# Kernel tuning notes

Hardware: AMD Instinct MI355X
Metric: run time of the kernel (lower is better)

The kernel has to match this reference:

```python
import jax, jax.numpy as jnp
import numpy as np

EPS_VAR = 1e-10
EPS_PERP = 1e-07


def setup_inputs() -> dict:
    key = jax.random.key(0)
    k1, k2 = jax.random.split(key, 2)
    bs, dim_z, W, H, K = 64, 64, 32, 32, 1024
    z_from_encoder = jax.random.normal(k1, (bs, dim_z, W, H), dtype=jnp.float32)
    codebook = jax.random.normal(k2, (K, dim_z), dtype=jnp.float32)
    var_q = jnp.ones((1,), dtype=jnp.float32)
    return {"z_from_encoder": z_from_encoder, "var_q": var_q, "codebook": codebook}


def _vq_forward(z_from_encoder, var_q, codebook):
    bs, dim_z, W, H = z_from_encoder.shape
    K = codebook.shape[0]
    # precision = 1 / clamp(var_q, min=1e-10); gaussian_1 -> global scalar weight
    precision_q = 1.0 / jnp.clip(var_q, EPS_VAR)
    weight = (0.5 * precision_q).reshape(())  # scalar

    # [bs, dim_z, W, H] -> [N, dim_z], N = bs*W*H
    z_flat = jnp.transpose(z_from_encoder, (0, 2, 3, 1)).reshape(-1, dim_z)

    # squared euclidean distance to every code: ||z||^2 + ||c||^2 - 2 z c^T  -> [N, K]
    d2 = (jnp.sum(z_flat * z_flat, axis=1, keepdims=True)
          + jnp.sum(codebook * codebook, axis=1)
          - 2.0 * (z_flat @ codebook.T))
    logit = -(weight * d2)

    log_probs = jax.nn.log_softmax(logit, axis=-1)   # [N, K]
    probs = jnp.exp(log_probs)                        # [N, K]

    # deterministic quantization: argmax -> gather codebook (== one_hot @ codebook)
    indices = jnp.argmax(logit, axis=1)               # [N]
    z_q = codebook[indices].reshape(bs, W, H, dim_z)
    z_to_decoder = jnp.transpose(z_q, (0, 3, 1, 2))   # [bs, dim_z, W, H]

    # avg_probs = mean of hard one-hot encodings (histogram of code usage)
    N = indices.shape[0]
    avg_probs = jnp.zeros((K,), dtype=logit.dtype).at[indices].add(1.0) / N

    # kld_discrete = sum(probs * log_probs) / bs  (sum over N and K)
    kld_discrete = jnp.sum(probs * log_probs) / bs
    # kld_continuous = mean over batch of sum_i weight * (z - z_q)^2
    diff2 = (z_from_encoder - z_to_decoder) ** 2
    kld_continuous = jnp.mean(jnp.sum(weight * diff2, axis=(1, 2, 3)))
    loss = kld_discrete + kld_continuous

    perplexity = jnp.exp(-jnp.sum(avg_probs * jnp.log(avg_probs + EPS_PERP)))
    return z_to_decoder, loss, perplexity


def reference(z_from_encoder, var_q, codebook):
    return _vq_forward(z_from_encoder, var_q, codebook)
```

## Files before the change

### kernel.cpp

```cpp
#include <hip/hip_runtime.h>

#define WS_CNORM_B  512
#define WS_COUNTS_B 4608
#define WS_CBHI_B   8704

typedef __attribute__((ext_vector_type(8))) short short8;
typedef __attribute__((ext_vector_type(4))) float f32x4;

__device__ __forceinline__ unsigned short f2bf(float x) {
  unsigned u = __builtin_bit_cast(unsigned, x);
  u += 0x7fffu + ((u >> 16) & 1u);
  return (unsigned short)(u >> 16);
}
__device__ __forceinline__ int qw(int r, int d) {
  return (r << 6) | (d ^ (r & 31));
}

__global__ __launch_bounds__(256) void vq_prep(const float* __restrict__ cb,
                                               char* __restrict__ ws) {
  int tid = blockIdx.x * 256 + threadIdx.x;
  unsigned* w32 = (unsigned*)ws;
  if (tid < 128) w32[tid] = 0u;
  if (tid < 1024) w32[1152 + tid] = 0u;
  int k = tid >> 6;
  float v = cb[tid];
  ((unsigned short*)(ws + WS_CBHI_B))[tid] = f2bf(v);
  float s = v * v;
  #pragma unroll
  for (int o = 32; o > 0; o >>= 1) s += __shfl_down(s, o);
  if ((threadIdx.x & 63) == 0) ((float*)(ws + WS_CNORM_B))[k] = s;
}

#define ST_OFF   16384
#define FIDX_OFF 17664

__global__ __launch_bounds__(256, 4) void vq_main(const float* __restrict__ z,
                                                  const float* __restrict__ cb,
                                                  const float* __restrict__ var_q,
                                                  char* __restrict__ ws,
                                                  float* __restrict__ out) {
  __shared__ __align__(16) char smem[17920];

  const int t = threadIdx.x;
  const int b = blockIdx.x;
  const int bb = b >> 4, p0 = (b & 15) << 6;
  const int l = t & 63, wv = t >> 6;
  const int lg = l >> 4, lr = l & 15;
  const float w = 0.5f / fmaxf(var_q[0], 1e-10f);
  const float w2 = 2.f * w;
  const float nw = -w;

  for (int i = 0; i < 8; ++i) {
    int idx = t + i * 256;
    int d2 = idx >> 6, p = idx & 63;
    float v0 = z[bb * 65536 + (2 * d2) * 1024 + p0 + p];
    float v1 = z[bb * 65536 + (2 * d2 + 1) * 1024 + p0 + p];
    unsigned short h0 = f2bf(v0), h1 = f2bf(v1);
    int byte = (p * 128 + d2 * 4) ^ ((p & 7) << 4);
    *(unsigned*)(smem + byte) = ((unsigned)h1 << 16) | h0;
  }
  __syncthreads();

  short8 a_hi[2];
  {
    int row = wv * 16 + lr;
    #pragma unroll
    for (int ks = 0; ks < 2; ++ks) {
      int byte = (row * 128 + ks * 64 + lg * 16) ^ ((row & 7) << 4);
      a_hi[ks] = *(const short8*)(smem + byte);
    }
  }
  __syncthreads();

  const char* cbh = ws + WS_CBHI_B;
  {
    #pragma unroll
    for (int pas = 0; pas < 2; ++pas) {
      int o = t + pas * 256;
      int dst = (o * 16) ^ (((o >> 3) & 7) << 4);
      *(f32x4*)(smem + dst) = *(const f32x4*)(cbh + o * 16);
    }
  }
  __syncthreads();

  float m[4], S1[4], S2[4], b1[4], b2[4];
  #pragma unroll
  for (int j = 0; j < 4; ++j) {
    m[j] = -1e30f; S1[j] = 0.f; S2[j] = 0.f; b1[j] = -1e30f; b2[j] = -1e30f;
  }

  const float* cnf = (const float*)(ws + WS_CNORM_B);

  for (int ch = 0; ch < 16; ++ch) {
    char* cur = smem + (ch & 1) * 8192;
    char* nxt = smem + ((ch + 1) & 1) * 8192;
    f32x4 rh0, rh1;
    const bool pf = ch < 15;
    if (pf) {
      const char* sh = cbh + (ch + 1) * 8192 + t * 16;
      rh0 = *(const f32x4*)sh;
      rh1 = *(const f32x4*)(sh + 4096);
    }
    float cn2[4];
    #pragma unroll
    for (int ct = 0; ct < 4; ++ct) cn2[ct] = nw * cnf[ch * 64 + ct * 16 + lr];

    f32x4 acc[4];
    #pragma unroll
    for (int ct = 0; ct < 4; ++ct) {
      f32x4 a = {};
      #pragma unroll
      for (int ks = 0; ks < 2; ++ks) {
        int cr = ct * 16 + lr;
        int byte = (cr * 128 + ks * 64 + lg * 16) ^ ((cr & 7) << 4);
        short8 bh = *(const short8*)(cur + byte);
        a = __builtin_amdgcn_mfma_f32_16x16x32_bf16(a_hi[ks], bh, a, 0, 0, 0);
      }
      acc[ct] = a;
    }

    #pragma unroll
    for (int j = 0; j < 4; ++j) {
      float lv[4];
      #pragma unroll
      for (int ct = 0; ct < 4; ++ct) lv[ct] = fmaf(acc[ct][j], w2, cn2[ct]);
      float lm = fmaxf(fmaxf(lv[0], lv[1]), fmaxf(lv[2], lv[3]));
      float mn = fmaxf(m[j], lm);
      float sc = __expf(m[j] - mn);
      S1[j] *= sc; S2[j] *= sc; m[j] = mn;
      #pragma unroll
      for (int ct = 0; ct < 4; ++ct) {
        float x = lv[ct];
        unsigned ku = (unsigned)(ch * 64 + ct * 16 + lr);
        unsigned xb = (__builtin_bit_cast(unsigned, x) & ~1023u) | ku;
        float xp = __builtin_bit_cast(float, xb);
        float tm = fminf(b1[j], xp);
        b1[j] = fmaxf(b1[j], xp);
        b2[j] = fmaxf(b2[j], tm);
        float e = __expf(x - mn);
        S1[j] += e;
        S2[j] = fmaf(x, e, S2[j]);
      }
    }

    if (pf) {
      #pragma unroll
      for (int pas = 0; pas < 2; ++pas) {
        int o = t + pas * 256;
        int dst = (o * 16) ^ (((o >> 3) & 7) << 4);
        *(f32x4*)(nxt + dst) = pas ? rh1 : rh0;
      }
    }
    __syncthreads();
  }

  #pragma unroll
  for (int st = 1; st < 16; st <<= 1) {
    #pragma unroll
    for (int j = 0; j < 4; ++j) {
      float om = __shfl_xor(m[j], st);
      float o1 = __shfl_xor(S1[j], st);
      float o2 = __shfl_xor(S2[j], st);
      float ov1 = __shfl_xor(b1[j], st);
      float ov2 = __shfl_xor(b2[j], st);
      float mn = fmaxf(m[j], om);
      float sa = __expf(m[j] - mn), sb = __expf(om - mn);
      S1[j] = sa * S1[j] + sb * o1;
      S2[j] = sa * S2[j] + sb * o2;
      m[j] = mn;
      float nb1 = fmaxf(b1[j], ov1);
      float nb2 = fmaxf(fminf(b1[j], ov1), fmaxf(b2[j], ov2));
      b1[j] = nb1; b2[j] = nb2;
    }
  }

  float* stw = (float*)(smem + ST_OFF);
  if (lr == 0) {
    #pragma unroll
    for (int j = 0; j < 4; ++j) {
      int r = wv * 16 + lg * 4 + j;
      float* p = stw + r * 5;
      p[0] = m[j]; p[1] = S1[j]; p[2] = S2[j]; p[3] = b1[j]; p[4] = b2[j];
    }
  }
  __syncthreads();

  int* fidx = (int*)(smem + FIDX_OFF);
  float rowent = 0.f, d2min = 0.f;
  if (t < 64) {
    const float* p = stw + t * 5;
    float mn = p[0], s1 = p[1], s2 = p[2];
    int ka = (int)(__builtin_bit_cast(unsigned, p[3]) & 1023u);
    int kb = (int)(__builtin_bit_cast(unsigned, p[4]) & 1023u);
    rowent = (s2 - mn * s1) / s1 - __logf(s1);
    const float* zp = z + bb * 65536 + p0 + t;
    const float* c1p = cb + ka * 64;
    const float* c2p = cb + kb * 64;
    float zn = 0.f, d1 = 0.f, d2 = 0.f;
    #pragma unroll 4
    for (int d4 = 0; d4 < 16; ++d4) {
      f32x4 ca = *(const f32x4*)(c1p + d4 * 4);
      f32x4 cc = *(const f32x4*)(c2p + d4 * 4);
      #pragma unroll
      for (int e = 0; e < 4; ++e) {
        float v = zp[(d4 * 4 + e) * 1024];
        zn = fmaf(v, v, zn);
        d1 = fmaf(v, ca[e], d1);
        d2 = fmaf(v, cc[e], d2);
      }
    }
    float da = zn + cnf[ka] - 2.f * d1;
    float db = zn + cnf[kb] - 2.f * d2;
    int kwin; float dwin;
    if (da < db || (da == db && ka < kb)) { kwin = ka; dwin = da; }
    else { kwin = kb; dwin = db; }
    fidx[t] = kwin;
    d2min = dwin;
    atomicAdd((unsigned*)(ws + WS_COUNTS_B) + kwin, 1u);
  }
  #pragma unroll
  for (int o = 32; o > 0; o >>= 1) {
    rowent += __shfl_down(rowent, o);
    d2min += __shfl_down(d2min, o);
  }
  if (t == 0) {
    float* wsf = (float*)ws;
    int slot = b & 63;
    atomicAdd(&wsf[slot * 2], rowent);
    atomicAdd(&wsf[slot * 2 + 1], d2min);
  }
  __syncthreads();

  float* zl = (float*)smem;
  for (int i = 0; i < 16; ++i) {
    int idx = t + i * 256;
    int r = idx >> 6, d = idx & 63;
    zl[qw(r, d)] = cb[fidx[r] * 64 + d];
  }
  __syncthreads();
  float* outz = out + bb * 65536 + p0;
  #pragma unroll
  for (int i = 0; i < 4; ++i) {
    int q = t + i * 256;
    int d = q >> 4, rq = q & 15, r = rq << 2;
    f32x4 v;
    v.x = zl[qw(r + 0, d)];
    v.y = zl[qw(r + 1, d)];
    v.z = zl[qw(r + 2, d)];
    v.w = zl[qw(r + 3, d)];
    *(f32x4*)&outz[d * 1024 + r] = v;
  }
}

__global__ __launch_bounds__(1024) void vq_finalize(const float* __restrict__ var_q,
                                                    char* __restrict__ ws,
                                                    float* __restrict__ out) {
  __shared__ float red[48];
  int t = threadIdx.x;
  const unsigned* counts = (const unsigned*)(ws + WS_COUNTS_B);
  const float* wsf = (const float*)ws;
  float avg = (float)counts[t] * (1.0f / 65536.0f);
  float term = avg * __logf(avg + 1e-7f);
  float pd = 0.f, pc = 0.f;
  if (t < 64) { pd = wsf[2 * t]; pc = wsf[2 * t + 1]; }
  #pragma unroll
  for (int o = 32; o > 0; o >>= 1) {
    term += __shfl_down(term, o);
    pd += __shfl_down(pd, o);
    pc += __shfl_down(pc, o);
  }
  int wv = t >> 6, lane = t & 63;
  if (lane == 0) { red[wv * 3] = term; red[wv * 3 + 1] = pd; red[wv * 3 + 2] = pc; }
  __syncthreads();
  if (t == 0) {
    float ts = 0.f, ps = 0.f, cs = 0.f;
    #pragma unroll
    for (int i = 0; i < 16; ++i) {
      ts += red[i * 3]; ps += red[i * 3 + 1]; cs += red[i * 3 + 2];
    }
    float w = 0.5f / fmaxf(var_q[0], 1e-10f);
    out[4194304] = ps / 64.f + w * cs / 64.f;
    out[4194305] = __expf(-ts);
  }
}

extern "C" void kernel_launch(void* const* d_in, const int* in_sizes, int n_in,
                              void* d_out, int out_size, void* d_ws, size_t ws_size,
                              hipStream_t stream) {
  const float* z = (const float*)d_in[0];
  const float* vq = (const float*)d_in[1];
  const float* cb = (const float*)d_in[2];
  float* out = (float*)d_out;
  char* ws = (char*)d_ws;

  vq_prep<<<256, 256, 0, stream>>>(cb, ws);
  vq_main<<<1024, 256, 0, stream>>>(z, cb, vq, ws, out);
  vq_finalize<<<1, 1024, 0, stream>>>(vq, ws, out);
}
```

Before: 58.12 us.

## Split codebook across two half-blocks of 512 threads and merge softmax stats

Doubles the block size to 512 threads. Each half of the block scans half of the codebook (512 codes) for the same 64 pixels, using its own double-buffered shared-memory region. The online-softmax and top-2 statistics from the two halves are merged at the end. This halves the serial chunk loop per block and adds parallelism, at the cost of twice the shared memory per block, an extra merge step, and tighter register limits from launch_bounds(512,8).

```diff
diff --git a/kernel.cpp b/kernel.cpp
--- a/kernel.cpp
+++ b/kernel.cpp
@@ -31,27 +31,29 @@
   if ((threadIdx.x & 63) == 0) ((float*)(ws + WS_CNORM_B))[k] = s;
 }
 
-#define ST_OFF   16384
-#define FIDX_OFF 17664
-
-__global__ __launch_bounds__(256, 4) void vq_main(const float* __restrict__ z,
+#define ST_OFF   32768
+#define FIDX_OFF 35328
+
+__global__ __launch_bounds__(512, 8) void vq_main(const float* __restrict__ z,
                                                   const float* __restrict__ cb,
                                                   const float* __restrict__ var_q,
                                                   char* __restrict__ ws,
                                                   float* __restrict__ out) {
-  __shared__ __align__(16) char smem[17920];
+  __shared__ __align__(16) char smem[35584];
 
   const int t = threadIdx.x;
   const int b = blockIdx.x;
   const int bb = b >> 4, p0 = (b & 15) << 6;
-  const int l = t & 63, wv = t >> 6;
+  const int half = t >> 8, th = t & 255;
+  const int wv = t >> 6, wq = wv & 3;
+  const int l = t & 63;
   const int lg = l >> 4, lr = l & 15;
   const float w = 0.5f / fmaxf(var_q[0], 1e-10f);
   const float w2 = 2.f * w;
   const float nw = -w;
 
-  for (int i = 0; i < 8; ++i) {
-    int idx = t + i * 256;
+  for (int i = 0; i < 4; ++i) {
+    int idx = t + i * 512;
     int d2 = idx >> 6, p = idx & 63;
     float v0 = z[bb * 65536 + (2 * d2) * 1024 + p0 + p];
     float v1 = z[bb * 65536 + (2 * d2 + 1) * 1024 + p0 + p];
@@ -63,7 +65,7 @@
 
   short8 a_hi[2];
   {
-    int row = wv * 16 + lr;
+    int row = wq * 16 + lr;
     #pragma unroll
     for (int ks = 0; ks < 2; ++ks) {
       int byte = (row * 128 + ks * 64 + lg * 16) ^ ((row & 7) << 4);
@@ -72,13 +74,14 @@
   }
   __syncthreads();
 
-  const char* cbh = ws + WS_CBHI_B;
+  const char* cbh = ws + WS_CBHI_B + half * 65536;
+  char* hbase = smem + half * 16384;
   {
     #pragma unroll
     for (int pas = 0; pas < 2; ++pas) {
-      int o = t + pas * 256;
+      int o = th + pas * 256;
       int dst = (o * 16) ^ (((o >> 3) & 7) << 4);
-      *(f32x4*)(smem + dst) = *(const f32x4*)(cbh + o * 16);
+      *(f32x4*)(hbase + dst) = *(const f32x4*)(cbh + o * 16);
     }
   }
   __syncthreads();
@@ -91,19 +94,20 @@
 
   const float* cnf = (const float*)(ws + WS_CNORM_B);
 
-  for (int ch = 0; ch < 16; ++ch) {
-    char* cur = smem + (ch & 1) * 8192;
-    char* nxt = smem + ((ch + 1) & 1) * 8192;
+  for (int ch = 0; ch < 8; ++ch) {
+    char* cur = hbase + (ch & 1) * 8192;
+    char* nxt = hbase + ((ch + 1) & 1) * 8192;
     f32x4 rh0, rh1;
-    const bool pf = ch < 15;
+    const bool pf = ch < 7;
     if (pf) {
-      const char* sh = cbh + (ch + 1) * 8192 + t * 16;
+      const char* sh = cbh + (ch + 1) * 8192 + th * 16;
       rh0 = *(const f32x4*)sh;
       rh1 = *(const f32x4*)(sh + 4096);
     }
     float cn2[4];
     #pragma unroll
-    for (int ct = 0; ct < 4; ++ct) cn2[ct] = nw * cnf[ch * 64 + ct * 16 + lr];
+    for (int ct = 0; ct < 4; ++ct)
+      cn2[ct] = nw * cnf[half * 512 + ch * 64 + ct * 16 + lr];
 
     f32x4 acc[4];
     #pragma unroll
@@ -131,7 +135,7 @@
       #pragma unroll
       for (int ct = 0; ct < 4; ++ct) {
         float x = lv[ct];
-        unsigned ku = (unsigned)(ch * 64 + ct * 16 + lr);
+        unsigned ku = (unsigned)(half * 512 + ch * 64 + ct * 16 + lr);
         unsigned xb = (__builtin_bit_cast(unsigned, x) & ~1023u) | ku;
         float xp = __builtin_bit_cast(float, xb);
         float tm = fminf(b1[j], xp);
@@ -146,7 +150,7 @@
     if (pf) {
       #pragma unroll
       for (int pas = 0; pas < 2; ++pas) {
-        int o = t + pas * 256;
+        int o = th + pas * 256;
         int dst = (o * 16) ^ (((o >> 3) & 7) << 4);
         *(f32x4*)(nxt + dst) = pas ? rh1 : rh0;
       }
@@ -178,8 +182,8 @@
   if (lr == 0) {
     #pragma unroll
     for (int j = 0; j < 4; ++j) {
-      int r = wv * 16 + lg * 4 + j;
-      float* p = stw + r * 5;
+      int r = wq * 16 + lg * 4 + j;
+      float* p = stw + (half * 64 + r) * 5;
       p[0] = m[j]; p[1] = S1[j]; p[2] = S2[j]; p[3] = b1[j]; p[4] = b2[j];
     }
   }
@@ -188,10 +192,18 @@
   int* fidx = (int*)(smem + FIDX_OFF);
   float rowent = 0.f, d2min = 0.f;
   if (t < 64) {
-    const float* p = stw + t * 5;
-    float mn = p[0], s1 = p[1], s2 = p[2];
-    int ka = (int)(__builtin_bit_cast(unsigned, p[3]) & 1023u);
-    int kb = (int)(__builtin_bit_cast(unsigned, p[4]) & 1023u);
+    const float* pA = stw + t * 5;
+    const float* pB = stw + (64 + t) * 5;
+    float mA = pA[0], s1A = pA[1], s2A = pA[2], a1 = pA[3], a2 = pA[4];
+    float mB = pB[0], s1B = pB[1], s2B = pB[2], c1 = pB[3], c2 = pB[4];
+    float mn = fmaxf(mA, mB);
+    float sa = __expf(mA - mn), sb = __expf(mB - mn);
+    float s1 = sa * s1A + sb * s1B;
+    float s2 = sa * s2A + sb * s2B;
+    float mb1 = fmaxf(a1, c1);
+    float mb2 = fmaxf(fminf(a1, c1), fmaxf(a2, c2));
+    int ka = (int)(__builtin_bit_cast(unsigned, mb1) & 1023u);
+    int kb = (int)(__builtin_bit_cast(unsigned, mb2) & 1023u);
     rowent = (s2 - mn * s1) / s1 - __logf(s1);
     const float* zp = z + bb * 65536 + p0 + t;
     const float* c1p = cb + ka * 64;
@@ -232,16 +244,16 @@
   __syncthreads();
 
   float* zl = (float*)smem;
-  for (int i = 0; i < 16; ++i) {
-    int idx = t + i * 256;
+  for (int i = 0; i < 8; ++i) {
+    int idx = t + i * 512;
     int r = idx >> 6, d = idx & 63;
     zl[qw(r, d)] = cb[fidx[r] * 64 + d];
   }
   __syncthreads();
   float* outz = out + bb * 65536 + p0;
   #pragma unroll
-  for (int i = 0; i < 4; ++i) {
-    int q = t + i * 256;
+  for (int i = 0; i < 2; ++i) {
+    int q = t + i * 512;
     int d = q >> 4, rq = q & 15, r = rq << 2;
     f32x4 v;
     v.x = zl[qw(r + 0, d)];
@@ -294,6 +306,6 @@
   char* ws = (char*)d_ws;
 
   vq_prep<<<256, 256, 0, stream>>>(cb, ws);
-  vq_main<<<1024, 256, 0, stream>>>(z, cb, vq, ws, out);
+  vq_main<<<1024, 512, 0, stream>>>(z, cb, vq, ws, out);
   vq_finalize<<<1, 1024, 0, stream>>>(vq, ws, out);
 }
```

New measurement: 102.8 us (median of 2 runs). 76.9% more time.
